# Optimization experiments

Measured on AMD Instinct MI355X. Metric: run time of the kernel, lower is better.

## Reference

```python
import jax, jax.numpy as jnp
import numpy as np

def setup_inputs() -> dict:
    key = jax.random.key(0)
    k1, k2 = jax.random.split(key)
    B, S, D, R = 16, 1024, 1024, 128
    batch = jax.random.normal(k1, (B, S, D), dtype=jnp.float32)
    # probe parameter initialized uniform(-0.05, 0.05) as in the torch module
    proj = jax.random.uniform(k2, (D, R), dtype=jnp.float32, minval=-0.05, maxval=0.05)
    return {"batch": batch, "proj": proj}

def reference(batch, proj):
    # transformed: [B, S, R]
    t = jnp.matmul(batch, proj)
    # squared L2 distances for all pairs: ||t_i||^2 + ||t_j||^2 - 2 t_i . t_j
    sq_norms = jnp.sum(t * t, axis=-1)                      # [B, S]
    cross = jnp.einsum('bir,bjr->bij', t, t)                # [B, S, S]
    d = sq_norms[:, :, None] + sq_norms[:, None, :] - 2.0 * cross
    return jnp.maximum(d, 0.0)  # clamp tiny negative values from the identity
```

## Files before the change

kernel.cpp:

```cpp
#include <hip/hip_runtime.h>

typedef __attribute__((ext_vector_type(8))) __bf16 bf16x8;
typedef __attribute__((ext_vector_type(4))) float f32x4;

#define B_ 16
#define S_ 1024
#define D_ 1024
#define R_ 128

__global__ __launch_bounds__(256) void k_transpose(const float* __restrict__ proj,
                                                   __bf16* __restrict__ projT) {
    __shared__ __bf16 tile[64][66];
    const int k0 = blockIdx.x * 64;
    const int r0 = blockIdx.y * 64;
#pragma unroll
    for (int it = 0; it < 16; ++it) {
        int idx = it * 256 + threadIdx.x;
        int kk = idx >> 6, rr = idx & 63;
        tile[kk][rr] = (__bf16)proj[(size_t)(k0 + kk) * R_ + (r0 + rr)];
    }
    __syncthreads();
#pragma unroll
    for (int it = 0; it < 16; ++it) {
        int idx = it * 256 + threadIdx.x;
        int rr = idx >> 6, kk = idx & 63;
        projT[(size_t)(r0 + rr) * D_ + (k0 + kk)] = tile[kk][rr];
    }
}

__global__ __launch_bounds__(256, 4) void k_proj(const float* __restrict__ batch,
                                                 const __bf16* __restrict__ projT,
                                                 __bf16* __restrict__ t,
                                                 float* __restrict__ sqn) {
    const int wave = threadIdx.x >> 6;
    const int lane = threadIdx.x & 63;
    const int ln = lane & 15;
    const int q  = lane >> 4;
    const int m0 = blockIdx.x * 16;
    const int kbase = wave * 256;
    const float* arow = batch + (size_t)(m0 + ln) * D_ + kbase;

    f32x4 acc[8];
#pragma unroll
    for (int ni = 0; ni < 8; ++ni) acc[ni] = f32x4{0.f, 0.f, 0.f, 0.f};

#pragma unroll 4
    for (int k0 = 0; k0 < 256; k0 += 32) {
        const int ka = k0 + q * 8;
        float4 alo = *(const float4*)(arow + ka);
        float4 ahi = *(const float4*)(arow + ka + 4);
        bf16x8 af;
        af[0] = (__bf16)alo.x; af[1] = (__bf16)alo.y;
        af[2] = (__bf16)alo.z; af[3] = (__bf16)alo.w;
        af[4] = (__bf16)ahi.x; af[5] = (__bf16)ahi.y;
        af[6] = (__bf16)ahi.z; af[7] = (__bf16)ahi.w;
#pragma unroll
        for (int ni = 0; ni < 8; ++ni) {
            bf16x8 bf = *(const bf16x8*)(projT + (size_t)(ni * 16 + ln) * D_ + kbase + ka);
            acc[ni] = __builtin_amdgcn_mfma_f32_16x16x32_bf16(af, bf, acc[ni], 0, 0, 0);
        }
    }

    __shared__ f32x4 red[4][8][64];
    __shared__ float sqpart[4][16];
#pragma unroll
    for (int ni = 0; ni < 8; ++ni) red[wave][ni][lane] = acc[ni];
    __syncthreads();

    float sq[4] = {0.f, 0.f, 0.f, 0.f};
#pragma unroll
    for (int p = 0; p < 2; ++p) {
        const int ni = wave * 2 + p;
        f32x4 v = red[0][ni][lane];
#pragma unroll
        for (int w = 1; w < 4; ++w) {
            f32x4 u = red[w][ni][lane];
            v[0] += u[0]; v[1] += u[1]; v[2] += u[2]; v[3] += u[3];
        }
#pragma unroll
        for (int r = 0; r < 4; ++r) {
            __bf16 h = (__bf16)v[r];
            t[(size_t)(m0 + q * 4 + r) * R_ + ni * 16 + ln] = h;
            float f = (float)h;
            sq[r] += f * f;
        }
    }
#pragma unroll
    for (int r = 0; r < 4; ++r) {
#pragma unroll
        for (int off = 1; off < 16; off <<= 1)
            sq[r] += __shfl_xor(sq[r], off, 64);
    }
    if (ln == 0) {
#pragma unroll
        for (int r = 0; r < 4; ++r) sqpart[wave][q * 4 + r] = sq[r];
    }
    __syncthreads();
    if (threadIdx.x < 16) {
        float s = sqpart[0][threadIdx.x] + sqpart[1][threadIdx.x] +
                  sqpart[2][threadIdx.x] + sqpart[3][threadIdx.x];
        sqn[m0 + threadIdx.x] = s;
    }
}

__global__ __launch_bounds__(256) void k_gram(const __bf16* __restrict__ t,
                                              const float* __restrict__ sqn,
                                              float* __restrict__ out) {
    const int b = blockIdx.z;
    const int wave = threadIdx.x >> 6;
    const int lane = threadIdx.x & 63;
    const int ln = lane & 15;
    const int q  = lane >> 4;
    const int wi = wave >> 1, wj = wave & 1;
    const int i0 = blockIdx.y * 128 + wi * 64;
    const int j0 = blockIdx.x * 128 + wj * 64;
    const __bf16* tb = t + (size_t)b * S_ * R_;
    const float* sqb = sqn + (size_t)b * S_;

    f32x4 acc[4][4];
#pragma unroll
    for (int mi = 0; mi < 4; ++mi)
#pragma unroll
        for (int ni = 0; ni < 4; ++ni) acc[mi][ni] = f32x4{0.f, 0.f, 0.f, 0.f};

#pragma unroll
    for (int k0 = 0; k0 < R_; k0 += 32) {
        const int ka = k0 + q * 8;
        bf16x8 af[4], bfm[4];
#pragma unroll
        for (int mi = 0; mi < 4; ++mi)
            af[mi] = *(const bf16x8*)(tb + (size_t)(i0 + mi * 16 + ln) * R_ + ka);
#pragma unroll
        for (int ni = 0; ni < 4; ++ni)
            bfm[ni] = *(const bf16x8*)(tb + (size_t)(j0 + ni * 16 + ln) * R_ + ka);
#pragma unroll
        for (int mi = 0; mi < 4; ++mi)
#pragma unroll
            for (int ni = 0; ni < 4; ++ni)
                acc[mi][ni] = __builtin_amdgcn_mfma_f32_16x16x32_bf16(
                    af[mi], bfm[ni], acc[mi][ni], 0, 0, 0);
    }

    float sqj[4];
#pragma unroll
    for (int ni = 0; ni < 4; ++ni) sqj[ni] = sqb[j0 + ni * 16 + ln];

    float* outb = out + (size_t)b * S_ * S_;
#pragma unroll
    for (int mi = 0; mi < 4; ++mi) {
#pragma unroll
        for (int r = 0; r < 4; ++r) {
            const int i = i0 + mi * 16 + q * 4 + r;
            const float si = sqb[i];
            float* orow = outb + (size_t)i * S_ + j0;
#pragma unroll
            for (int ni = 0; ni < 4; ++ni) {
                float v = si + sqj[ni] - 2.f * acc[mi][ni][r];
                orow[ni * 16 + ln] = fmaxf(v, 0.f);
            }
        }
    }
}

extern "C" void kernel_launch(void* const* d_in, const int* in_sizes, int n_in,
                              void* d_out, int out_size, void* d_ws, size_t ws_size,
                              hipStream_t stream) {
    const float* batch = (const float*)d_in[0];
    const float* proj  = (const float*)d_in[1];
    float* out = (float*)d_out;

    char* ws = (char*)d_ws;
    __bf16* t     = (__bf16*)ws;
    __bf16* projT = (__bf16*)(ws + (size_t)B_ * S_ * R_ * 2);
    float*  sqn   = (float*)(ws + (size_t)B_ * S_ * R_ * 2
                                + (size_t)R_ * D_ * 2);

    k_transpose<<<dim3(D_ / 64, R_ / 64), 256, 0, stream>>>(proj, projT);
    k_proj<<<dim3((B_ * S_) / 16), 256, 0, stream>>>(batch, projT, t, sqn);
    k_gram<<<dim3(S_ / 128, S_ / 128, B_), 256, 0, stream>>>(t, sqn, out);
}
```

Before: 157.0 us.

## Stage operands through swizzled LDS via direct global-to-LDS loads in projection and gram kernels

The projection kernel now splits the output N dimension across waves instead of splitting K. It streams A (fp32 batch rows) and the bf16 projT tiles into swizzled, double-buffered LDS using global_load_lds, which removes the cross-wave reduction through shared memory. The gram kernel loads its full 128x128 i/j tiles of t into swizzled LDS once, so waves share them instead of each issuing redundant global loads. This adds LDS usage and block-level barriers, and occupancy is limited to 2 blocks per CU for gram.

```diff
diff --git a/kernel.cpp b/kernel.cpp
--- a/kernel.cpp
+++ b/kernel.cpp
@@ -2,11 +2,17 @@
 
 typedef __attribute__((ext_vector_type(8))) __bf16 bf16x8;
 typedef __attribute__((ext_vector_type(4))) float f32x4;
+typedef const __attribute__((address_space(1))) unsigned int gu32;
+typedef __attribute__((address_space(3))) unsigned int lu32;
 
 #define B_ 16
 #define S_ 1024
 #define D_ 1024
 #define R_ 128
+
+__device__ __forceinline__ void gl16(const void* g, void* l) {
+    __builtin_amdgcn_global_load_lds((gu32*)g, (lu32*)l, 16, 0, 0);
+}
 
 __global__ __launch_bounds__(256) void k_transpose(const float* __restrict__ proj,
                                                    __bf16* __restrict__ projT) {
@@ -32,51 +38,73 @@
                                                  const __bf16* __restrict__ projT,
                                                  __bf16* __restrict__ t,
                                                  float* __restrict__ sqn) {
+    __shared__ __align__(16) char smem[40960];
     const int wave = threadIdx.x >> 6;
     const int lane = threadIdx.x & 63;
-    const int ln = lane & 15;
-    const int q  = lane >> 4;
+    const int ln = lane & 15, q = lane >> 4;
     const int m0 = blockIdx.x * 16;
-    const int kbase = wave * 256;
-    const float* arow = batch + (size_t)(m0 + ln) * D_ + kbase;
-
-    f32x4 acc[8];
-#pragma unroll
-    for (int ni = 0; ni < 8; ++ni) acc[ni] = f32x4{0.f, 0.f, 0.f, 0.f};
-
-#pragma unroll 4
-    for (int k0 = 0; k0 < 256; k0 += 32) {
-        const int ka = k0 + q * 8;
-        float4 alo = *(const float4*)(arow + ka);
-        float4 ahi = *(const float4*)(arow + ka + 4);
-        bf16x8 af;
-        af[0] = (__bf16)alo.x; af[1] = (__bf16)alo.y;
-        af[2] = (__bf16)alo.z; af[3] = (__bf16)alo.w;
-        af[4] = (__bf16)ahi.x; af[5] = (__bf16)ahi.y;
-        af[6] = (__bf16)ahi.z; af[7] = (__bf16)ahi.w;
-#pragma unroll
-        for (int ni = 0; ni < 8; ++ni) {
-            bf16x8 bf = *(const bf16x8*)(projT + (size_t)(ni * 16 + ln) * D_ + kbase + ka);
-            acc[ni] = __builtin_amdgcn_mfma_f32_16x16x32_bf16(af, bf, acc[ni], 0, 0, 0);
-        }
-    }
-
-    __shared__ f32x4 red[4][8][64];
-    __shared__ float sqpart[4][16];
-#pragma unroll
-    for (int ni = 0; ni < 8; ++ni) red[wave][ni][lane] = acc[ni];
-    __syncthreads();
-
+
+    const int arow = wave * 4 + (lane >> 4);
+    const int aswz = ((arow & 7) << 5) | ((arow & 8) << 1);
+    const char* ag = (const char*)batch + (size_t)(m0 + arow) * 4096
+                   + (((lane & 15) * 16) ^ aswz);
+    const int brx = wave * 8 + (lane >> 3);
+    const int bswz = (brx & 7) << 4;
+    const char* bg = (const char*)projT + (size_t)brx * 2048
+                   + (((lane & 7) * 16) ^ bswz);
+    char* const abuf0 = smem + wave * 1024;
+    char* const bbuf0 = smem + 8192 + wave * 1024;
+
+    const int raswz = ((ln & 7) << 5) | ((ln & 8) << 1);
+    const int rbswz = (ln & 7) << 4;
+    const int kq = q * 32;
+    const int kq2 = q * 16;
+
+    f32x4 acc[2];
+    acc[0] = f32x4{0.f, 0.f, 0.f, 0.f};
+    acc[1] = f32x4{0.f, 0.f, 0.f, 0.f};
+
+    gl16(ag, abuf0);
+#pragma unroll
+    for (int s = 0; s < 4; ++s) gl16(bg + (size_t)s * 65536, bbuf0 + s * 4096);
+    __syncthreads();
+
+#pragma unroll 2
+    for (int c = 0; c < 16; ++c) {
+        const int cur = c & 1, nxt = cur ^ 1;
+        if (c < 15) {
+            gl16(ag + (c + 1) * 256, abuf0 + nxt * 4096);
+#pragma unroll
+            for (int s = 0; s < 4; ++s)
+                gl16(bg + (size_t)s * 65536 + (c + 1) * 128,
+                     bbuf0 + nxt * 16384 + s * 4096);
+        }
+        const char* ab = smem + cur * 4096 + ln * 256;
+        const char* bb = smem + 8192 + cur * 16384 + ln * 128;
+#pragma unroll
+        for (int ks = 0; ks < 2; ++ks) {
+            float4 lo = *(const float4*)(ab + ((ks * 128 + kq) ^ raswz));
+            float4 hi = *(const float4*)(ab + ((ks * 128 + kq + 16) ^ raswz));
+            bf16x8 af;
+            af[0] = (__bf16)lo.x; af[1] = (__bf16)lo.y;
+            af[2] = (__bf16)lo.z; af[3] = (__bf16)lo.w;
+            af[4] = (__bf16)hi.x; af[5] = (__bf16)hi.y;
+            af[6] = (__bf16)hi.z; af[7] = (__bf16)hi.w;
+            const int ko = (ks * 64 + kq2) ^ rbswz;
+            bf16x8 bf0 = *(const bf16x8*)(bb + (wave * 2 + 0) * 2048 + ko);
+            bf16x8 bf1 = *(const bf16x8*)(bb + (wave * 2 + 1) * 2048 + ko);
+            acc[0] = __builtin_amdgcn_mfma_f32_16x16x32_bf16(af, bf0, acc[0], 0, 0, 0);
+            acc[1] = __builtin_amdgcn_mfma_f32_16x16x32_bf16(af, bf1, acc[1], 0, 0, 0);
+        }
+        __syncthreads();
+    }
+
+    float* sqpart = (float*)smem;
     float sq[4] = {0.f, 0.f, 0.f, 0.f};
 #pragma unroll
     for (int p = 0; p < 2; ++p) {
         const int ni = wave * 2 + p;
-        f32x4 v = red[0][ni][lane];
-#pragma unroll
-        for (int w = 1; w < 4; ++w) {
-            f32x4 u = red[w][ni][lane];
-            v[0] += u[0]; v[1] += u[1]; v[2] += u[2]; v[3] += u[3];
-        }
+        f32x4 v = acc[p];
 #pragma unroll
         for (int r = 0; r < 4; ++r) {
             __bf16 h = (__bf16)v[r];
@@ -93,46 +121,63 @@
     }
     if (ln == 0) {
 #pragma unroll
-        for (int r = 0; r < 4; ++r) sqpart[wave][q * 4 + r] = sq[r];
+        for (int r = 0; r < 4; ++r) sqpart[wave * 16 + q * 4 + r] = sq[r];
     }
     __syncthreads();
     if (threadIdx.x < 16) {
-        float s = sqpart[0][threadIdx.x] + sqpart[1][threadIdx.x] +
-                  sqpart[2][threadIdx.x] + sqpart[3][threadIdx.x];
+        float s = sqpart[threadIdx.x] + sqpart[16 + threadIdx.x] +
+                  sqpart[32 + threadIdx.x] + sqpart[48 + threadIdx.x];
         sqn[m0 + threadIdx.x] = s;
     }
 }
 
-__global__ __launch_bounds__(256) void k_gram(const __bf16* __restrict__ t,
-                                              const float* __restrict__ sqn,
-                                              float* __restrict__ out) {
+__global__ __launch_bounds__(256, 2) void k_gram(const __bf16* __restrict__ t,
+                                                 const float* __restrict__ sqn,
+                                                 float* __restrict__ out) {
+    __shared__ __align__(16) char smem[65536];
     const int b = blockIdx.z;
-    const int wave = threadIdx.x >> 6;
-    const int lane = threadIdx.x & 63;
-    const int ln = lane & 15;
-    const int q  = lane >> 4;
+    const int wave = threadIdx.x >> 6, lane = threadIdx.x & 63;
+    const int ln = lane & 15, q = lane >> 4;
     const int wi = wave >> 1, wj = wave & 1;
-    const int i0 = blockIdx.y * 128 + wi * 64;
-    const int j0 = blockIdx.x * 128 + wj * 64;
+    const int i0b = blockIdx.y * 128, j0b = blockIdx.x * 128;
     const __bf16* tb = t + (size_t)b * S_ * R_;
     const float* sqb = sqn + (size_t)b * S_;
 
+    const int grow = wave * 4 + (lane >> 4);
+    const int gwin = ((lane & 15) * 16) ^ ((grow & 7) << 4);
+    const char* agt = (const char*)tb + (size_t)(i0b + grow) * 256 + gwin;
+    const char* bgt = (const char*)tb + (size_t)(j0b + grow) * 256 + gwin;
+    char* const adst = smem + wave * 1024;
+    char* const bdst = smem + 32768 + wave * 1024;
+#pragma unroll
+    for (int s = 0; s < 8; ++s) gl16(agt + (size_t)s * 4096, adst + s * 4096);
+#pragma unroll
+    for (int s = 0; s < 8; ++s) gl16(bgt + (size_t)s * 4096, bdst + s * 4096);
+
+    float sqj[4];
+#pragma unroll
+    for (int ni = 0; ni < 4; ++ni) sqj[ni] = sqb[j0b + wj * 64 + ni * 16 + ln];
+    __syncthreads();
+
     f32x4 acc[4][4];
 #pragma unroll
     for (int mi = 0; mi < 4; ++mi)
 #pragma unroll
         for (int ni = 0; ni < 4; ++ni) acc[mi][ni] = f32x4{0.f, 0.f, 0.f, 0.f};
 
-#pragma unroll
-    for (int k0 = 0; k0 < R_; k0 += 32) {
-        const int ka = k0 + q * 8;
+    const int rsw = (ln & 7) << 4;
+    const char* abA = smem + (size_t)(wi * 64 + ln) * 256;
+    const char* abB = smem + 32768 + (size_t)(wj * 64 + ln) * 256;
+#pragma unroll
+    for (int ks = 0; ks < 4; ++ks) {
+        const int ko = (ks * 64 + q * 16) ^ rsw;
         bf16x8 af[4], bfm[4];
 #pragma unroll
         for (int mi = 0; mi < 4; ++mi)
-            af[mi] = *(const bf16x8*)(tb + (size_t)(i0 + mi * 16 + ln) * R_ + ka);
+            af[mi] = *(const bf16x8*)(abA + mi * 4096 + ko);
 #pragma unroll
         for (int ni = 0; ni < 4; ++ni)
-            bfm[ni] = *(const bf16x8*)(tb + (size_t)(j0 + ni * 16 + ln) * R_ + ka);
+            bfm[ni] = *(const bf16x8*)(abB + ni * 4096 + ko);
 #pragma unroll
         for (int mi = 0; mi < 4; ++mi)
 #pragma unroll
@@ -141,10 +186,7 @@
                     af[mi], bfm[ni], acc[mi][ni], 0, 0, 0);
     }
 
-    float sqj[4];
-#pragma unroll
-    for (int ni = 0; ni < 4; ++ni) sqj[ni] = sqb[j0 + ni * 16 + ln];
-
+    const int i0 = i0b + wi * 64, j0 = j0b + wj * 64;
     float* outb = out + (size_t)b * S_ * S_;
 #pragma unroll
     for (int mi = 0; mi < 4; ++mi) {
```

New measurement: 141.5 us. -9.9%, faster.
